# Kernel tuning notes

Measured on AMD Instinct MI355X. Metric: run time of the kernel, lower is better.

## Reference

```python
import jax, jax.numpy as jnp
import numpy as np

NU, NI, D, E = 100000, 50000, 128, 500000


def setup_inputs() -> dict:
    key = jax.random.key(0)
    ks = jax.random.split(key, 10)
    s = 1.0 / np.sqrt(D)
    return {
        "feat_user": jax.random.normal(ks[0], (NU, D), jnp.float32),
        "feat_item": jax.random.normal(ks[1], (NI, D), jnp.float32),
        "W1": jax.random.normal(ks[2], (D, D), jnp.float32) * s,
        "b1": jnp.zeros((D,), jnp.float32),
        "W2": jax.random.normal(ks[3], (D, D), jnp.float32) * s,
        "b2": jnp.zeros((D,), jnp.float32),
        "norm_u2i": jax.random.uniform(ks[4], (E, 1), jnp.float32),
        "norm_i2u": jax.random.uniform(ks[5], (E, 1), jnp.float32),
        "edge_u2i_src": jax.random.randint(ks[6], (E,), 0, NU, jnp.int32),
        "edge_u2i_dst": jax.random.randint(ks[7], (E,), 0, NI, jnp.int32),
        "edge_i2u_src": jax.random.randint(ks[8], (E,), 0, NI, jnp.int32),
        "edge_i2u_dst": jax.random.randint(ks[9], (E,), 0, NU, jnp.int32),
    }


def reference(feat_user, feat_item, W1, b1, W2, b2, norm_u2i, norm_i2u,
              edge_u2i_src, edge_u2i_dst, edge_i2u_src, edge_i2u_dst):
    lin1 = lambda x: x @ W1 + b1
    lin2 = lambda x: x @ W2 + b2

    # self-loop etypes: copy_u(W1(feat)) summed over one self-edge per node
    h_user = lin1(feat_user)
    h_item = lin1(feat_item)

    # user -> item edges: norm * (W1(e_u) + W2(e_u * e_i)), scatter-sum to items
    su = feat_user[edge_u2i_src]            # [E, D]
    di = feat_item[edge_u2i_dst]            # [E, D]
    m_ui = norm_u2i * (lin1(su) + lin2(su * di))
    h_item = h_item + jax.ops.segment_sum(m_ui, edge_u2i_dst, num_segments=feat_item.shape[0])

    # item -> user edges
    si = feat_item[edge_i2u_src]
    du = feat_user[edge_i2u_dst]
    m_iu = norm_i2u * (lin1(si) + lin2(si * du))
    h_user = h_user + jax.ops.segment_sum(m_iu, edge_i2u_dst, num_segments=feat_user.shape[0])

    def finish(h):
        h = jax.nn.leaky_relu(h, 0.2)       # LeakyReLU(0.2); dropout p=0 is identity
        n = jnp.linalg.norm(h, axis=1, keepdims=True)
        return h / jnp.maximum(n, 1e-12)    # F.normalize(dim=1, p=2), eps=1e-12

    return finish(h_user), finish(h_item)
```

## Files before the change

kernel.cpp:

```cpp
#include <hip/hip_runtime.h>

#define DD 128
#define SCAN_TILE 1024
#define HS 132
#define FR 16

typedef __attribute__((ext_vector_type(8))) short short8;
typedef __attribute__((ext_vector_type(4))) float f32x4;

__device__ inline unsigned short f2bf_rne(float f) {
    unsigned int u = __float_as_uint(f);
    unsigned int r = u + 0x7FFFu + ((u >> 16) & 1u);
    return (unsigned short)(r >> 16);
}
__device__ inline float bf2f(unsigned short h) {
    return __uint_as_float(((unsigned int)h) << 16);
}
__device__ inline void split2(float a, float b, unsigned int& hi, unsigned int& lo) {
    unsigned short ha = f2bf_rne(a), hb = f2bf_rne(b);
    float la = a - bf2f(ha), lb = b - bf2f(hb);
    hi = (unsigned int)ha | ((unsigned int)hb << 16);
    lo = (unsigned int)f2bf_rne(la) | ((unsigned int)f2bf_rne(lb) << 16);
}

__global__ __launch_bounds__(256) void count_wprep_kernel(
    const int* __restrict__ dst1, int E1, int* deg1,
    const int* __restrict__ dst2, int E2, int* deg2,
    const float* __restrict__ W1, const float* __restrict__ W2,
    unsigned short* wfrag)
{
    int b = blockIdx.x;
    if (b < 16) {
        int t = b * 256 + threadIdx.x;
        int lane = t & 63;
        int cf   = (t >> 6) & 7;
        int ksm  = (t >> 9) & 3;
        int mat  = t >> 11;
        const float* W = mat ? W2 : W1;
        int g = lane >> 4, c = lane & 15;
        int n = cf * 16 + c;
        unsigned int hi[4], lo[4];
        #pragma unroll
        for (int p = 0; p < 4; ++p) {
            int k0 = ksm * 32 + g * 8 + p * 2;
            float v0 = W[(size_t)k0 * DD + n];
            float v1 = W[(size_t)(k0 + 1) * DD + n];
            split2(v0, v1, hi[p], lo[p]);
        }
        unsigned short* dh = wfrag + (size_t)mat * 32768
                           + ((size_t)(ksm * 8 + cf) * 64 + lane) * 8;
        unsigned short* dl = dh + 16384;
        *(uint4*)dh = make_uint4(hi[0], hi[1], hi[2], hi[3]);
        *(uint4*)dl = make_uint4(lo[0], lo[1], lo[2], lo[3]);
        return;
    }
    int t = (b - 16) * 256 + threadIdx.x;
    if (t < E1) {
        atomicAdd(deg1 + dst1[t], 1);
    } else if (t - E1 < E2) {
        atomicAdd(deg2 + dst2[t - E1], 1);
    }
}

__global__ __launch_bounds__(256) void scanA_kernel(
    const int* __restrict__ cur_i, int NI,
    const int* __restrict__ cur_u, int NU,
    int* bsum, int nb0)
{
    int b = blockIdx.x;
    const int* cur;
    int N, base;
    if (b < nb0) { cur = cur_i; N = NI; base = b * SCAN_TILE; }
    else         { cur = cur_u; N = NU; base = (b - nb0) * SCAN_TILE; }
    int t = threadIdx.x;
    int idx0 = base + t * 4;
    int s = 0;
    #pragma unroll
    for (int k = 0; k < 4; ++k) {
        int idx = idx0 + k;
        if (idx < N) s += cur[idx];
    }
    __shared__ int red[256];
    red[t] = s;
    __syncthreads();
    for (int o = 128; o >= 1; o >>= 1) {
        if (t < o) red[t] += red[t + o];
        __syncthreads();
    }
    if (t == 0) bsum[b] = red[0];
}

__device__ int block_exscan_inplace(int* a, int n)
{
    __shared__ int sh[256];
    int t = threadIdx.x;
    int carry = 0;
    for (int base = 0; base < n; base += 256) {
        int v = (base + t < n) ? a[base + t] : 0;
        sh[t] = v;
        __syncthreads();
        for (int off = 1; off < 256; off <<= 1) {
            int u = (t >= off) ? sh[t - off] : 0;
            __syncthreads();
            sh[t] += u;
            __syncthreads();
        }
        if (base + t < n) a[base + t] = carry + sh[t] - v;
        int csum = sh[255];
        __syncthreads();
        carry += csum;
    }
    return carry;
}

__global__ __launch_bounds__(256) void scanB_kernel(
    int* bsum, int nb0, int nb1,
    int* row_i, int NI, int* row_u, int NU)
{
    int tot0 = block_exscan_inplace(bsum, nb0);
    __syncthreads();
    int tot1 = block_exscan_inplace(bsum + nb0, nb1);
    if (threadIdx.x == 0) {
        row_i[NI] = tot0;
        row_u[NU] = tot1;
    }
}

__global__ __launch_bounds__(256) void scanC_kernel(
    int* cur_i, int* row_i, int NI,
    int* cur_u, int* row_u, int NU,
    const int* __restrict__ bsum, int nb0)
{
    int b = blockIdx.x;
    int off = bsum[b];
    int* cur; int* row;
    int N, base;
    if (b < nb0) { cur = cur_i; row = row_i; N = NI; base = b * SCAN_TILE; }
    else         { cur = cur_u; row = row_u; N = NU; base = (b - nb0) * SCAN_TILE; }
    int t = threadIdx.x;
    int idx0 = base + t * 4;
    int v[4];
    int s = 0;
    #pragma unroll
    for (int k = 0; k < 4; ++k) {
        int idx = idx0 + k;
        v[k] = (idx < N) ? cur[idx] : 0;
        s += v[k];
    }
    __shared__ int sh[256];
    sh[t] = s;
    __syncthreads();
    for (int o = 1; o < 256; o <<= 1) {
        int u = (t >= o) ? sh[t - o] : 0;
        __syncthreads();
        sh[t] += u;
        __syncthreads();
    }
    int run = off + sh[t] - s;
    #pragma unroll
    for (int k = 0; k < 4; ++k) {
        int idx = idx0 + k;
        if (idx < N) {
            row[idx] = run;
            cur[idx] = run;
            run += v[k];
        }
    }
}

__global__ __launch_bounds__(256) void fill_pg_kernel(
    const int* __restrict__ dst1, const int* __restrict__ src1,
    const float* __restrict__ norm1, int E1, int* cur1, int2* esn1,
    const int* __restrict__ dst2, const int* __restrict__ src2,
    const float* __restrict__ norm2, int E2, int* cur2, int2* esn2)
{
    int t = blockIdx.x * 256 + threadIdx.x;
    if (t < E1) {
        int pos = atomicAdd(cur1 + dst1[t], 1);
        esn1[pos] = make_int2(src1[t], __float_as_int(norm1[t]));
    } else if (t - E1 < E2) {
        int e = t - E1;
        int pos = atomicAdd(cur2 + dst2[e], 1);
        esn2[pos] = make_int2(src2[e], __float_as_int(norm2[e]));
    }
}


__global__ __launch_bounds__(256) void scatter_kernel(
    const float* __restrict__ feat_src,
    const int* __restrict__ src,
    const int* __restrict__ dst,
    const float* __restrict__ norm,
    float* agg,
    float* ssum,
    int E)
{
    int gw = (int)((blockIdx.x * 256u + threadIdx.x) >> 6);
    int lane = threadIdx.x & 63;
    if (gw >= E) return;
    int si = src[gw];
    int di = dst[gw];
    float nv = norm[gw];
    float2 v = *(const float2*)(feat_src + (size_t)si * DD + lane * 2);
    float* ap = agg + (size_t)di * DD + lane * 2;
    unsafeAtomicAdd(ap,     v.x * nv);
    unsafeAtomicAdd(ap + 1, v.y * nv);
    if (lane == 0) unsafeAtomicAdd(ssum + di, nv);
}

__global__ __launch_bounds__(256) void fused_kernel(
    const float* __restrict__ feat_user, const float* __restrict__ feat_item,
    const int* __restrict__ row_u, const int2* __restrict__ esnU,
    int NU, int nbU,
    const int* __restrict__ row_i, const int2* __restrict__ esnI, int NI,
    const unsigned short* __restrict__ wfrag,
    const float* __restrict__ b1, const float* __restrict__ b2,
    float* out_base)
{
    __shared__ __align__(16) char smem[FR * 512 * 2];
    __shared__ float sst[FR];

    const float *featO, *featS;
    const int *row;
    const int2 *esn;
    float* out;
    int row0, nrows;
    if ((int)blockIdx.x < nbU) {
        featO = feat_user; featS = feat_item; row = row_u; esn = esnU;
        out = out_base; row0 = blockIdx.x * FR; nrows = NU;
    } else {
        featO = feat_item; featS = feat_user; row = row_i; esn = esnI;
        out = out_base + (size_t)NU * DD;
        row0 = (blockIdx.x - nbU) * FR; nrows = NI;
    }

    int t = threadIdx.x;
    int w = t >> 6;
    int lane = t & 63;
    char* pAh = smem;
    char* pAl = smem + FR * 512;

    for (int rr = 0; rr < 4; ++rr) {
        int r = w * 4 + rr;
        int grow = row0 + r;
        float2 acc = {0.f, 0.f};
        float sn = 0.f;
        float2 f2 = {0.f, 0.f};
        if (grow < nrows) {
            f2 = *(const float2*)(featO + (size_t)grow * DD + lane * 2);
            int beg = row[grow], end = row[grow + 1];
            int j = beg;
            for (; j + 4 <= end; j += 4) {
                int2 e0 = esn[j],     e1 = esn[j + 1];
                int2 e2 = esn[j + 2], e3 = esn[j + 3];
                float2 v0 = *(const float2*)(featS + (size_t)e0.x * DD + lane * 2);
                float2 v1 = *(const float2*)(featS + (size_t)e1.x * DD + lane * 2);
                float2 v2 = *(const float2*)(featS + (size_t)e2.x * DD + lane * 2);
                float2 v3 = *(const float2*)(featS + (size_t)e3.x * DD + lane * 2);
                float n0 = __int_as_float(e0.y), n1 = __int_as_float(e1.y);
                float n2 = __int_as_float(e2.y), n3 = __int_as_float(e3.y);
                acc.x += n0 * v0.x + n1 * v1.x + n2 * v2.x + n3 * v3.x;
                acc.y += n0 * v0.y + n1 * v1.y + n2 * v2.y + n3 * v3.y;
                sn += n0 + n1 + n2 + n3;
            }
            for (; j < end; ++j) {
                int2 e0 = esn[j];
                float n0 = __int_as_float(e0.y);
                float2 v0 = *(const float2*)(featS + (size_t)e0.x * DD + lane * 2);
                acc.x += n0 * v0.x;
                acc.y += n0 * v0.y;
                sn += n0;
            }
        }
        float x0 = f2.x + acc.x, x1 = f2.y + acc.y;
        float y0 = f2.x * acc.x, y1 = f2.y * acc.y;
        unsigned int xh, xl, yh, yl;
        split2(x0, x1, xh, xl);
        split2(y0, y1, yh, yl);
        int swz = (r & 7) << 4;
        int rb = r * 512;
        int xo = rb + ((4 * lane) ^ swz);
        int yo = rb + ((256 + 4 * lane) ^ swz);
        *(unsigned int*)(pAh + xo) = xh;
        *(unsigned int*)(pAl + xo) = xl;
        *(unsigned int*)(pAh + yo) = yh;
        *(unsigned int*)(pAl + yo) = yl;
        if (lane == 0) sst[r] = sn;
    }
    __syncthreads();

    int r16 = lane & 15, g = lane >> 4;
    f32x4 acc0 = {0.f,0.f,0.f,0.f}, acc1 = {0.f,0.f,0.f,0.f};
    const char* cAh = (const char*)pAh;
    const char* cAl = (const char*)pAl;
    int swzA = (r16 & 7) << 4;
    int ob0 = r16 * 512;

    #pragma unroll 2
    for (int ks = 0; ks < 8; ++ks) {
        int offx = (ks * 64 + g * 16) ^ swzA;
        short8 a0h = *(const short8*)(cAh + ob0 + offx);
        short8 a0l = *(const short8*)(cAl + ob0 + offx);
        int mat = ks >> 2, ksm = ks & 3;
        const unsigned short* ph = wfrag + (size_t)mat * 32768;
        const unsigned short* pl = ph + 16384;
        int bo0 = ((ksm * 8 + w * 2) * 64 + lane) * 8;
        int bo1 = bo0 + 512;
        short8 b0h = *(const short8*)(ph + bo0);
        short8 b0l = *(const short8*)(pl + bo0);
        short8 b1h = *(const short8*)(ph + bo1);
        short8 b1l = *(const short8*)(pl + bo1);
        acc0 = __builtin_amdgcn_mfma_f32_16x16x32_bf16(a0h, b0h, acc0, 0, 0, 0);
        acc0 = __builtin_amdgcn_mfma_f32_16x16x32_bf16(a0h, b0l, acc0, 0, 0, 0);
        acc0 = __builtin_amdgcn_mfma_f32_16x16x32_bf16(a0l, b0h, acc0, 0, 0, 0);
        acc1 = __builtin_amdgcn_mfma_f32_16x16x32_bf16(a0h, b1h, acc1, 0, 0, 0);
        acc1 = __builtin_amdgcn_mfma_f32_16x16x32_bf16(a0h, b1l, acc1, 0, 0, 0);
        acc1 = __builtin_amdgcn_mfma_f32_16x16x32_bf16(a0l, b1h, acc1, 0, 0, 0);
    }
    __syncthreads();

    float* hbuf = (float*)smem;
    #pragma unroll
    for (int j = 0; j < 4; ++j) {
        int rA = g * 4 + j;
        hbuf[rA * HS + (w * 32 + r16)]      = acc0[j];
        hbuf[rA * HS + (w * 32 + 16 + r16)] = acc1[j];
    }
    __syncthreads();

    int c0 = t & 63, c1 = c0 + 64, rg = t >> 6;
    float b1c0 = b1[c0], b1c1 = b1[c1];
    float b2c0 = b2[c0], b2c1 = b2[c1];
    #pragma unroll
    for (int rr = 0; rr < 4; ++rr) {
        int lr = rg * 4 + rr;
        int row_ = row0 + lr;
        if (row_ < nrows) {
            float s = sst[lr];
            float h0 = hbuf[lr * HS + c0] + (1.0f + s) * b1c0 + s * b2c0;
            float h1 = hbuf[lr * HS + c1] + (1.0f + s) * b1c1 + s * b2c1;
            h0 = h0 >= 0.f ? h0 : 0.2f * h0;
            h1 = h1 >= 0.f ? h1 : 0.2f * h1;
            float loc = h0 * h0 + h1 * h1;
            #pragma unroll
            for (int m = 32; m >= 1; m >>= 1) loc += __shfl_xor(loc, m, 64);
            float inv = 1.0f / fmaxf(sqrtf(loc), 1e-12f);
            __builtin_nontemporal_store(h0 * inv, out + (size_t)row_ * DD + c0);
            __builtin_nontemporal_store(h1 * inv, out + (size_t)row_ * DD + c1);
        }
    }
}


__global__ __launch_bounds__(256) void finish_kernel(
    const float* __restrict__ feat,
    const float* agg,
    const float* __restrict__ ssum,
    const float* __restrict__ W1,
    const float* __restrict__ b1,
    const float* __restrict__ W2,
    const float* __restrict__ b2,
    float* out,
    int nrows)
{
    __shared__ float xs[32][DD];
    __shared__ float ys[32][DD];
    int row0 = blockIdx.x * 32;
    int tid = threadIdx.x;

    for (int i = tid; i < 32 * (DD / 4); i += 256) {
        int r = i >> 5;
        int c4 = (i & 31) * 4;
        int row = row0 + r;
        if (row < nrows) {
            float4 f = *(const float4*)(feat + (size_t)row * DD + c4);
            float4 a = *(const float4*)(agg  + (size_t)row * DD + c4);
            float4 x, y;
            x.x = f.x + a.x; x.y = f.y + a.y; x.z = f.z + a.z; x.w = f.w + a.w;
            y.x = f.x * a.x; y.y = f.y * a.y; y.z = f.z * a.z; y.w = f.w * a.w;
            *(float4*)&xs[r][c4] = x;
            *(float4*)&ys[r][c4] = y;
        }
    }
    __syncthreads();

    int c0 = tid & 63;
    int rg = tid >> 6;
    int c1 = c0 + 64;

    float acc[8][2] = {{0.f,0.f},{0.f,0.f},{0.f,0.f},{0.f,0.f},
                       {0.f,0.f},{0.f,0.f},{0.f,0.f},{0.f,0.f}};
    for (int k = 0; k < DD; k += 4) {
        float w1a[4], w1b[4], w2a[4], w2b[4];
        #pragma unroll
        for (int kk = 0; kk < 4; ++kk) {
            const float* wr1 = W1 + (size_t)(k + kk) * DD;
            const float* wr2 = W2 + (size_t)(k + kk) * DD;
            w1a[kk] = wr1[c0]; w1b[kk] = wr1[c1];
            w2a[kk] = wr2[c0]; w2b[kk] = wr2[c1];
        }
        #pragma unroll
        for (int r = 0; r < 8; ++r) {
            float4 xv = *(const float4*)&xs[rg * 8 + r][k];
            float4 yv = *(const float4*)&ys[rg * 8 + r][k];
            acc[r][0] += xv.x*w1a[0] + xv.y*w1a[1] + xv.z*w1a[2] + xv.w*w1a[3]
                       + yv.x*w2a[0] + yv.y*w2a[1] + yv.z*w2a[2] + yv.w*w2a[3];
            acc[r][1] += xv.x*w1b[0] + xv.y*w1b[1] + xv.z*w1b[2] + xv.w*w1b[3]
                       + yv.x*w2b[0] + yv.y*w2b[1] + yv.z*w2b[2] + yv.w*w2b[3];
        }
    }

    float b1c0 = b1[c0], b1c1 = b1[c1];
    float b2c0 = b2[c0], b2c1 = b2[c1];

    #pragma unroll
    for (int r = 0; r < 8; ++r) {
        int row = row0 + rg * 8 + r;
        if (row < nrows) {
            float s = ssum[row];
            float h0 = acc[r][0] + (1.0f + s) * b1c0 + s * b2c0;
            float h1 = acc[r][1] + (1.0f + s) * b1c1 + s * b2c1;
            h0 = h0 >= 0.f ? h0 : 0.2f * h0;
            h1 = h1 >= 0.f ? h1 : 0.2f * h1;
            float loc = h0 * h0 + h1 * h1;
            #pragma unroll
            for (int m = 32; m >= 1; m >>= 1) loc += __shfl_xor(loc, m, 64);
            float inv = 1.0f / fmaxf(sqrtf(loc), 1e-12f);
            out[(size_t)row * DD + c0] = h0 * inv;
            out[(size_t)row * DD + c1] = h1 * inv;
        }
    }
}

extern "C" void kernel_launch(void* const* d_in, const int* in_sizes, int n_in,
                              void* d_out, int out_size, void* d_ws, size_t ws_size,
                              hipStream_t stream) {
    const float* feat_user = (const float*)d_in[0];
    const float* feat_item = (const float*)d_in[1];
    const float* W1        = (const float*)d_in[2];
    const float* b1        = (const float*)d_in[3];
    const float* W2        = (const float*)d_in[4];
    const float* b2        = (const float*)d_in[5];
    const float* norm_u2i  = (const float*)d_in[6];
    const float* norm_i2u  = (const float*)d_in[7];
    const int* eus = (const int*)d_in[8];
    const int* eud = (const int*)d_in[9];
    const int* eis = (const int*)d_in[10];
    const int* eid = (const int*)d_in[11];

    int NU = in_sizes[0] / DD;
    int NI = in_sizes[1] / DD;
    int E1 = in_sizes[8];
    int E2 = in_sizes[10];
    float* out = (float*)d_out;

    int nb0 = (NI + SCAN_TILE - 1) / SCAN_TILE;
    int nb1 = (NU + SCAN_TILE - 1) / SCAN_TILE;
    int nbU = (NU + FR - 1) / FR;
    int nbI = (NI + FR - 1) / FR;

    size_t wfrag_bytes = 131072;
    size_t need_pg   = wfrag_bytes + 64  +
                       ((size_t)3 * NU + 3 * NI + 2 * E1 + 2 * E2 + 2
                        + nb0 + nb1) * sizeof(int);

    int eb = (int)(((long long)E1 + E2 + 255) / 256);

    if (ws_size >= need_pg) {
        unsigned short* wfrag = (unsigned short*)d_ws;
        int* cur_i = (int*)((char*)d_ws + wfrag_bytes);
        int* cur_u = cur_i + NI;
        int* row_i = cur_u + NU;
        int* row_u = row_i + NI + 1;
        int* pend  = row_u + NU + 1;
        int2* esn1 = (int2*)(((uintptr_t)pend + 15) & ~(uintptr_t)15);
        int2* esn2 = esn1 + E1;
        int* bsum  = (int*)(esn2 + E2);

        hipMemsetAsync(cur_i, 0, (size_t)(NI + NU) * sizeof(int), stream);

        count_wprep_kernel<<<16 + eb, 256, 0, stream>>>(
            eud, E1, cur_i, eid, E2, cur_u, W1, W2, wfrag);
        scanA_kernel<<<nb0 + nb1, 256, 0, stream>>>(cur_i, NI, cur_u, NU,
                                                    bsum, nb0);
        scanB_kernel<<<1, 256, 0, stream>>>(bsum, nb0, nb1,
                                            row_i, NI, row_u, NU);
        scanC_kernel<<<nb0 + nb1, 256, 0, stream>>>(cur_i, row_i, NI,
                                                    cur_u, row_u, NU,
                                                    bsum, nb0);
        fill_pg_kernel<<<eb, 256, 0, stream>>>(
            eud, eus, norm_u2i, E1, cur_i, esn1,
            eid, eis, norm_i2u, E2, cur_u, esn2);

        fused_kernel<<<nbU + nbI, 256, 0, stream>>>(
            feat_user, feat_item,
            row_u, esn2, NU, nbU,
            row_i, esn1, NI,
            wfrag, b1, b2, out);
    } else {
        float* agg_user = out;
        float* agg_item = out + (size_t)NU * DD;
        float* s_user = (float*)d_ws;
        float* s_item = s_user + NU;

        hipMemsetAsync(out, 0, (size_t)out_size * sizeof(float), stream);
        hipMemsetAsync(d_ws, 0, (size_t)(NU + NI) * sizeof(float), stream);

        int b1n = (int)(((long long)E1 * 64 + 255) / 256);
        scatter_kernel<<<b1n, 256, 0, stream>>>(feat_user, eus, eud, norm_u2i,
                                                agg_item, s_item, E1);
        int b2n = (int)(((long long)E2 * 64 + 255) / 256);
        scatter_kernel<<<b2n, 256, 0, stream>>>(feat_item, eis, eid, norm_i2u,
                                                agg_user, s_user, E2);

        finish_kernel<<<(NU + 31) / 32, 256, 0, stream>>>(
            feat_user, agg_user, s_user, W1, b1, W2, b2, out, NU);
        finish_kernel<<<(NI + 31) / 32, 256, 0, stream>>>(
            feat_item, agg_item, s_item, W1, b1, W2, b2,
            out + (size_t)NU * DD, NI);
    }
}
```

Before: 379.6 us.

## Fold block-sum scan into scanC, deepen gather unroll, add occupancy hints

Removes the single-block scanB launch: every scanC block now loads all block sums (up to 512) into shared memory and scans them itself, which saves one kernel launch at the cost of redundant per-block work. The fused kernel's neighbor gather loop is unrolled from 4 to 6 edges with a 2-edge tail, and the self-feature read becomes a nontemporal load. It also adds launch_bounds(256,8) for occupancy and changes the HS padding constant. A guard falls back to the atomic path when more than 512 scan blocks are needed.

```diff
diff --git a/kernel.cpp b/kernel.cpp
--- a/kernel.cpp
+++ b/kernel.cpp
@@ -2,11 +2,12 @@
 
 #define DD 128
 #define SCAN_TILE 1024
-#define HS 132
+#define HS 136
 #define FR 16
 
 typedef __attribute__((ext_vector_type(8))) short short8;
 typedef __attribute__((ext_vector_type(4))) float f32x4;
+typedef __attribute__((ext_vector_type(2))) float f32x2;
 
 __device__ inline unsigned short f2bf_rne(float f) {
     unsigned int u = __float_as_uint(f);
@@ -90,54 +91,48 @@
     if (t == 0) bsum[b] = red[0];
 }
 
-__device__ int block_exscan_inplace(int* a, int n)
-{
-    __shared__ int sh[256];
-    int t = threadIdx.x;
-    int carry = 0;
-    for (int base = 0; base < n; base += 256) {
-        int v = (base + t < n) ? a[base + t] : 0;
-        sh[t] = v;
-        __syncthreads();
-        for (int off = 1; off < 256; off <<= 1) {
-            int u = (t >= off) ? sh[t - off] : 0;
-            __syncthreads();
-            sh[t] += u;
-            __syncthreads();
-        }
-        if (base + t < n) a[base + t] = carry + sh[t] - v;
-        int csum = sh[255];
-        __syncthreads();
-        carry += csum;
-    }
-    return carry;
-}
-
-__global__ __launch_bounds__(256) void scanB_kernel(
-    int* bsum, int nb0, int nb1,
-    int* row_i, int NI, int* row_u, int NU)
-{
-    int tot0 = block_exscan_inplace(bsum, nb0);
-    __syncthreads();
-    int tot1 = block_exscan_inplace(bsum + nb0, nb1);
-    if (threadIdx.x == 0) {
-        row_i[NI] = tot0;
-        row_u[NU] = tot1;
-    }
-}
-
 __global__ __launch_bounds__(256) void scanC_kernel(
     int* cur_i, int* row_i, int NI,
     int* cur_u, int* row_u, int NU,
-    const int* __restrict__ bsum, int nb0)
-{
+    const int* __restrict__ bsum, int nb0, int nb1)
+{
+    __shared__ int bs[512];
+    __shared__ int ps[256];
+    __shared__ int sh[256];
     int b = blockIdx.x;
-    int off = bsum[b];
+    int t = threadIdx.x;
+    int ntot = nb0 + nb1;
+
+    bs[t]       = (t < ntot)       ? bsum[t]       : 0;
+    bs[256 + t] = (256 + t < ntot) ? bsum[256 + t] : 0;
+    __syncthreads();
+    int b0v = bs[2 * t], b1v = bs[2 * t + 1];
+    int pair = b0v + b1v;
+    ps[t] = pair;
+    __syncthreads();
+    for (int o = 1; o < 256; o <<= 1) {
+        int u = (t >= o) ? ps[t - o] : 0;
+        __syncthreads();
+        ps[t] += u;
+        __syncthreads();
+    }
+    int e0 = ps[t] - pair;
+    __syncthreads();
+    bs[2 * t]     = e0;
+    bs[2 * t + 1] = e0 + b0v;
+    __syncthreads();
+    int grand = ps[255];
+    int totI  = bs[nb0];
+    if (b == 0 && t == 0) {
+        row_i[NI] = totI;
+        row_u[NU] = grand - totI;
+    }
+    int off = (b < nb0) ? bs[b] : bs[b] - totI;
+
     int* cur; int* row;
     int N, base;
     if (b < nb0) { cur = cur_i; row = row_i; N = NI; base = b * SCAN_TILE; }
     else         { cur = cur_u; row = row_u; N = NU; base = (b - nb0) * SCAN_TILE; }
-    int t = threadIdx.x;
     int idx0 = base + t * 4;
     int v[4];
     int s = 0;
@@ -147,7 +142,6 @@
         v[k] = (idx < N) ? cur[idx] : 0;
         s += v[k];
     }
-    __shared__ int sh[256];
     sh[t] = s;
     __syncthreads();
     for (int o = 1; o < 256; o <<= 1) {
@@ -208,7 +202,7 @@
     if (lane == 0) unsafeAtomicAdd(ssum + di, nv);
 }
 
-__global__ __launch_bounds__(256) void fused_kernel(
+__global__ __launch_bounds__(256, 8) void fused_kernel(
     const float* __restrict__ feat_user, const float* __restrict__ feat_item,
     const int* __restrict__ row_u, const int2* __restrict__ esnU,
     int NU, int nbU,
@@ -245,28 +239,45 @@
         int grow = row0 + r;
         float2 acc = {0.f, 0.f};
         float sn = 0.f;
-        float2 f2 = {0.f, 0.f};
+        f32x2 f2 = {0.f, 0.f};
         if (grow < nrows) {
-            f2 = *(const float2*)(featO + (size_t)grow * DD + lane * 2);
+            f2 = __builtin_nontemporal_load(
+                     (const f32x2*)(featO + (size_t)grow * DD + lane * 2));
             int beg = row[grow], end = row[grow + 1];
             int j = beg;
-            for (; j + 4 <= end; j += 4) {
-                int2 e0 = esn[j],     e1 = esn[j + 1];
-                int2 e2 = esn[j + 2], e3 = esn[j + 3];
-                float2 v0 = *(const float2*)(featS + (size_t)e0.x * DD + lane * 2);
-                float2 v1 = *(const float2*)(featS + (size_t)e1.x * DD + lane * 2);
-                float2 v2 = *(const float2*)(featS + (size_t)e2.x * DD + lane * 2);
-                float2 v3 = *(const float2*)(featS + (size_t)e3.x * DD + lane * 2);
+            for (; j + 6 <= end; j += 6) {
+                int2 e0 = esn[j],     e1 = esn[j + 1], e2 = esn[j + 2];
+                int2 e3 = esn[j + 3], e4 = esn[j + 4], e5 = esn[j + 5];
+                const float* fb = featS + lane * 2;
+                float2 v0 = *(const float2*)(fb + ((size_t)e0.x << 7));
+                float2 v1 = *(const float2*)(fb + ((size_t)e1.x << 7));
+                float2 v2 = *(const float2*)(fb + ((size_t)e2.x << 7));
+                float2 v3 = *(const float2*)(fb + ((size_t)e3.x << 7));
+                float2 v4 = *(const float2*)(fb + ((size_t)e4.x << 7));
+                float2 v5 = *(const float2*)(fb + ((size_t)e5.x << 7));
                 float n0 = __int_as_float(e0.y), n1 = __int_as_float(e1.y);
                 float n2 = __int_as_float(e2.y), n3 = __int_as_float(e3.y);
-                acc.x += n0 * v0.x + n1 * v1.x + n2 * v2.x + n3 * v3.x;
-                acc.y += n0 * v0.y + n1 * v1.y + n2 * v2.y + n3 * v3.y;
-                sn += n0 + n1 + n2 + n3;
+                float n4 = __int_as_float(e4.y), n5 = __int_as_float(e5.y);
+                acc.x += n0 * v0.x + n1 * v1.x + n2 * v2.x
+                       + n3 * v3.x + n4 * v4.x + n5 * v5.x;
+                acc.y += n0 * v0.y + n1 * v1.y + n2 * v2.y
+                       + n3 * v3.y + n4 * v4.y + n5 * v5.y;
+                sn += n0 + n1 + n2 + n3 + n4 + n5;
             }
-            for (; j < end; ++j) {
+            for (; j + 2 <= end; j += 2) {
+                int2 e0 = esn[j], e1 = esn[j + 1];
+                const float* fb = featS + lane * 2;
+                float2 v0 = *(const float2*)(fb + ((size_t)e0.x << 7));
+                float2 v1 = *(const float2*)(fb + ((size_t)e1.x << 7));
+                float n0 = __int_as_float(e0.y), n1 = __int_as_float(e1.y);
+                acc.x += n0 * v0.x + n1 * v1.x;
+                acc.y += n0 * v0.y + n1 * v1.y;
+                sn += n0 + n1;
+            }
+            if (j < end) {
                 int2 e0 = esn[j];
                 float n0 = __int_as_float(e0.y);
-                float2 v0 = *(const float2*)(featS + (size_t)e0.x * DD + lane * 2);
+                float2 v0 = *(const float2*)(featS + ((size_t)e0.x << 7) + lane * 2);
                 acc.x += n0 * v0.x;
                 acc.y += n0 * v0.y;
                 sn += n0;
@@ -466,7 +477,7 @@
 
     int eb = (int)(((long long)E1 + E2 + 255) / 256);
 
-    if (ws_size >= need_pg) {
+    if (ws_size >= need_pg && nb0 + nb1 <= 512) {
         unsigned short* wfrag = (unsigned short*)d_ws;
         int* cur_i = (int*)((char*)d_ws + wfrag_bytes);
         int* cur_u = cur_i + NI;
@@ -483,11 +494,9 @@
             eud, E1, cur_i, eid, E2, cur_u, W1, W2, wfrag);
         scanA_kernel<<<nb0 + nb1, 256, 0, stream>>>(cur_i, NI, cur_u, NU,
                                                     bsum, nb0);
-        scanB_kernel<<<1, 256, 0, stream>>>(bsum, nb0, nb1,
-                                            row_i, NI, row_u, NU);
         scanC_kernel<<<nb0 + nb1, 256, 0, stream>>>(cur_i, row_i, NI,
                                                     cur_u, row_u, NU,
-                                                    bsum, nb0);
+                                                    bsum, nb0, nb1);
         fill_pg_kernel<<<eb, 256, 0, stream>>>(
             eud, eus, norm_u2i, E1, cur_i, esn1,
             eid, eis, norm_i2u, E2, cur_u, esn2);
```

New measurement: 374.1 us. No clear change (-1.5%).
